# Kernel tuning notes

Hardware: AMD Instinct MI355X
Metric: run time of the kernel (lower is better)

## Reference

```python
import jax, jax.numpy as jnp
import numpy as np

B, N, K = 4, 1024, 512
HEADS, DH = 8, 64
HID = 2048
KAPPA = 1.0      # kappa_beta
ALPHA = 1e-3     # ffn_alpha (prior weight)
LAM = 1.0        # ffn_lambda_belief
NITER = 2        # ffn_n_iterations
EPS = 1e-8


def _ln(x, g, b):
    m = jnp.mean(x, axis=-1, keepdims=True)
    v = jnp.var(x, axis=-1, keepdims=True)
    return (x - m) * jax.lax.rsqrt(v + 1e-5) * g + b


def _transport(x, phi, G):
    # truncated exp(phi . G) applied to x without materializing (B,N,K,K)
    def Ax(y):
        return jnp.einsum('bng,gkl,bnl->bnk', phi, G, y)
    a1 = Ax(x)
    return x + a1 + 0.5 * Ax(a1)


def setup_inputs() -> dict:
    key = jax.random.key(0)
    ks = jax.random.split(key, 16)
    mu_q = jax.random.normal(ks[0], (B, N, K), dtype=jnp.float32)
    sigma_q = jax.random.uniform(ks[1], (B, N, K), minval=0.5, maxval=1.5, dtype=jnp.float32)
    phi = 0.1 * jax.random.normal(ks[2], (B, N, 3), dtype=jnp.float32)
    A = jax.random.normal(ks[3], (3, K, K), dtype=jnp.float32)
    generators = 0.05 * (A - jnp.transpose(A, (0, 2, 1)))  # antisymmetric Lie generators
    mask = jnp.broadcast_to(jnp.tril(jnp.ones((N, N), dtype=bool)), (B, N, N))  # causal
    mu_prior = jax.random.normal(ks[4], (B, N, K), dtype=jnp.float32)
    s = 0.02
    Wq = s * jax.random.normal(ks[5], (K, K), dtype=jnp.float32)
    Wk = s * jax.random.normal(ks[6], (K, K), dtype=jnp.float32)
    Wv = s * jax.random.normal(ks[7], (K, K), dtype=jnp.float32)
    Wo = s * jax.random.normal(ks[8], (K, K), dtype=jnp.float32)
    g1 = jnp.ones((K,), jnp.float32); be1 = jnp.zeros((K,), jnp.float32)
    g2 = jnp.ones((K,), jnp.float32); be2 = jnp.zeros((K,), jnp.float32)
    W1 = s * jax.random.normal(ks[9], (K, HID), dtype=jnp.float32)
    bh1 = jnp.zeros((HID,), jnp.float32)
    W2 = s * jax.random.normal(ks[10], (HID, K), dtype=jnp.float32)
    bh2 = jnp.zeros((K,), jnp.float32)
    lr = jnp.array(0.1, jnp.float32)  # learnable VFE step size
    return {'mu_q': mu_q, 'sigma_q': sigma_q, 'phi': phi, 'generators': generators,
            'mask': mask, 'mu_prior': mu_prior, 'Wq': Wq, 'Wk': Wk, 'Wv': Wv, 'Wo': Wo,
            'g1': g1, 'be1': be1, 'g2': g2, 'be2': be2,
            'W1': W1, 'bh1': bh1, 'W2': W2, 'bh2': bh2, 'lr': lr}


def reference(mu_q, sigma_q, phi, generators, mask, mu_prior,
              Wq, Wk, Wv, Wo, g1, be1, g2, be2, W1, bh1, W2, bh2, lr):
    # ---- attention sublayer ----
    mu_n = _ln(mu_q, g1, be1)
    mu_g = _transport(mu_n, phi, generators)  # transport to common frame

    def heads(x):  # (B,N,K) -> (B,H,N,Dh)
        return x.reshape(B, N, HEADS, DH).transpose(0, 2, 1, 3)

    q = heads(mu_g @ Wq)
    k = heads(mu_g @ Wk)
    v = heads(mu_g @ Wv)
    # diagonal covariance propagated through linear maps: var_out = sigma @ W^2
    sq = heads(sigma_q @ (Wq * Wq)) + EPS
    sk = heads(sigma_q @ (Wk * Wk)) + EPS

    inv = 1.0 / sq
    # KL(N(k_j,sk_j) || N(q_i,sq_i)) for diagonal Gaussians, decomposed into matmuls
    tr = jnp.einsum('bhid,bhjd->bhij', inv, sk)
    quad = (jnp.sum(q * q * inv, axis=-1)[..., None]
            - 2.0 * jnp.einsum('bhid,bhjd->bhij', q * inv, k)
            + jnp.einsum('bhid,bhjd->bhij', inv, k * k))
    logdet = (jnp.sum(jnp.log(sq), axis=-1)[..., None]
              - jnp.sum(jnp.log(sk), axis=-1)[:, :, None, :])
    kl = 0.5 * (tr + quad - DH + logdet)  # (B,H,N,N)

    scores = jnp.where(mask[:, None, :, :], -kl / KAPPA, -1e9)
    beta = jax.nn.softmax(scores, axis=-1)

    out = jnp.einsum('bhij,bhjd->bhid', beta, v)
    out = out.transpose(0, 2, 1, 3).reshape(B, N, K)
    mu_attn = _transport(out @ Wo, -phi, generators)  # back-transport to local frames
    mu_res = mu_q + mu_attn  # residual (dropout is identity in eval)

    # ---- VFE_dynamic FFN sublayer ----
    mu_n2 = _ln(mu_res, g2, be2)
    beta_m = jnp.mean(beta, axis=1)  # (B,N,N) attention-belief coupling
    h = mu_n2
    for _ in range(NITER):
        drive = jax.nn.gelu(h @ W1 + bh1) @ W2 + bh2
        grad = ALPHA * (h - mu_prior) + LAM * (h - jnp.einsum('bij,bjk->bik', beta_m, h))
        h = h + lr * (drive - grad)
    mu_out = mu_res + (h - mu_n2)

    return (mu_out, sigma_q, phi)
```

## Files before the change

kernel.cpp:

```cpp
#include <hip/hip_runtime.h>
#include <math.h>

#define BB 4
#define NN 1024
#define KK 512
#define HH 8
#define DHh 64
#define HIDd 2048
#define BN (BB*NN)

typedef unsigned short u16;
typedef __attribute__((ext_vector_type(8))) short bf16x8;
typedef __attribute__((ext_vector_type(4))) float f32x4;

__device__ __forceinline__ float gelu_tanh(float x){
    float u = 0.7978845608028654f*(x + 0.044715f*x*x*x);
    u = fminf(fmaxf(u, -15.f), 15.f);
    float t = __expf(2.f*u);
    return x*t/(t+1.f);
}
__device__ __forceinline__ u16 f2bf(float x){
    unsigned int u = __float_as_uint(x);
    unsigned int r = (u + 0x7fffu + ((u>>16)&1u)) >> 16;
    return (u16)r;
}
__device__ __forceinline__ float bf2f(u16 b){
    return __uint_as_float(((unsigned int)b)<<16);
}
__device__ __forceinline__ void gload16(const void* g, void* l){
    __builtin_amdgcn_global_load_lds((__attribute__((address_space(1))) void*)g,
                                     (__attribute__((address_space(3))) void*)l, 16, 0, 0);
}
__device__ __forceinline__ void wsplit(u16* hi, u16* lo, size_t o, float v){
    u16 h = f2bf(v);
    hi[o] = h;
    if (lo) lo[o] = f2bf(v - bf2f(h));
}

__global__ __launch_bounds__(256) void split_t_k(
    const float* __restrict__ src, u16* __restrict__ hi, u16* __restrict__ lo,
    int Kc, int Nc, long sS, long sD, int square)
{
    __shared__ float t[32][33];
    const int n0 = blockIdx.x*32, k0 = blockIdx.y*32, bz = blockIdx.z;
    const float* S = src + (long)bz*sS;
    const int tx = threadIdx.x & 31, ty = threadIdx.x >> 5;
    for (int r = ty; r < 32; r += 8){
        float v = S[(long)(k0+r)*Nc + n0+tx];
        if (square) v *= v;
        t[r][tx] = v;
    }
    __syncthreads();
    for (int r = ty; r < 32; r += 8){
        float v = t[tx][r];
        long o = (long)bz*sD + (long)(n0+r)*Kc + k0 + tx;
        wsplit(hi, lo, o, v);
    }
}

__global__ __launch_bounds__(256) void wmega_k(
    const float* __restrict__ Wq, const float* __restrict__ Wk,
    const float* __restrict__ Wv, const float* __restrict__ Wo,
    const float* __restrict__ W1, const float* __restrict__ W2,
    const float* __restrict__ gen,
    u16* __restrict__ WQKVh, u16* __restrict__ WQKVl, u16* __restrict__ WoTh,
    u16* __restrict__ WSQKh, u16* __restrict__ WSQKl,
    u16* __restrict__ W1Th, u16* __restrict__ W2Th, u16* __restrict__ GFh)
{
    const int z = blockIdx.z;
    const int tid = threadIdx.x;
    if (z == 8){
        if (blockIdx.x >= 48) return;
        const int c0 = blockIdx.x*32, k0 = blockIdx.y*32;
        const int tx = tid&31, ty = tid>>5;
        const int g = c0/KK, l0 = c0%KK;
        for (int r=ty; r<32; r+=8)
            GFh[(size_t)(k0+r)*(3*KK) + c0+tx] =
                f2bf(gen[(size_t)g*KK*KK + (size_t)(k0+r)*KK + l0+tx]);
        return;
    }
    __shared__ float t[32][33];
    const float* src; u16* hi; u16* lo=0; int sq=0;
    int n0, k0, Kc, Nc;
    const size_t KK2 = (size_t)KK*KK;
    if (z < 6){
        if (blockIdx.x >= 16) return;
        n0 = blockIdx.x*32; k0 = blockIdx.y*32; Kc=KK; Nc=KK;
        if      (z==0){ src=Wq; hi=WQKVh;       lo=WQKVl; }
        else if (z==1){ src=Wk; hi=WQKVh+KK2;   lo=WQKVl+KK2; }
        else if (z==2){ src=Wv; hi=WQKVh+2*KK2; lo=WQKVl+2*KK2; }
        else if (z==3){ src=Wo; hi=WoTh; }
        else if (z==4){ src=Wq; hi=WSQKh;       lo=WSQKl; sq=1; }
        else          { src=Wk; hi=WSQKh+KK2;   lo=WSQKl+KK2; sq=1; }
    } else if (z == 6){
        src=W1; hi=W1Th; Kc=KK; Nc=HIDd;
        n0 = blockIdx.x*32; k0 = blockIdx.y*32;
    } else {
        src=W2; hi=W2Th; Kc=HIDd; Nc=KK;
        n0 = blockIdx.y*32; k0 = blockIdx.x*32;
    }
    const int tx=tid&31, ty=tid>>5;
    for (int r=ty;r<32;r+=8){
        float v = src[(long)(k0+r)*Nc + n0+tx];
        if (sq) v*=v;
        t[r][tx]=v;
    }
    __syncthreads();
    for (int r=ty;r<32;r+=8){
        float v = t[tx][r];
        long o = (long)(n0+r)*Kc + k0+tx;
        wsplit(hi, lo, o, v);
    }
}

__global__ __launch_bounds__(256) void gemm_mfma_k(
    const u16* __restrict__ Ah, const u16* __restrict__ Bh,
    float* __restrict__ C, u16* __restrict__ Chi, u16* __restrict__ Clo,
    int M, int Kc, int Nc, int lda,
    long sA, long sB, long sC, const float* __restrict__ bias, int act,
    int swz,
    const u16* __restrict__ A2, const u16* __restrict__ B2,
    float* __restrict__ C2, int ycut)
{
    __shared__ u16 shA[3][128*32], shB[3][128*32];
    int bx = blockIdx.x, by = blockIdx.y;
    if (swz){
        int lin = bx + gridDim.x*by;
        int within = lin & 31, st = lin >> 5;
        int stm = gridDim.x >> 3;
        bx = (st % stm)*8 + (within & 7);
        by = (st / stm)*4 + (within >> 3);
    }
    int bz = blockIdx.z;
    int m0, n0, kend;
    const u16 *gAh, *gBh;
    if (ycut && by < ycut){
        m0 = (bx & 7)*128; n0 = by*128; bz = bx >> 3;
        gAh = A2 + (long)bz*NN*NN;
        gBh = B2 + (long)bz*KK*NN;
        Kc = NN; lda = NN; Nc = KK;
        C = C2 + (long)bz*NN*KK; Chi = 0; Clo = 0; bias = 0; act = 0; sC = 0;
        kend = m0 + 128;
        bz = 0;
    } else {
        if (ycut) by -= ycut;
        m0 = bx*128; n0 = by*128;
        gAh = Ah + (long)bz*sA;
        gBh = Bh + (long)bz*sB;
        kend = Kc;
    }
    const int tid = threadIdx.x;
    const int wave = tid >> 6, lane = tid & 63;
    const int quad = lane >> 4, r16 = lane & 15;
    const int wm = (wave>>1)*64, wn = (wave&1)*64;

    f32x4 acc[4][4];
    #pragma unroll
    for (int i=0;i<4;i++)
        #pragma unroll
        for (int j=0;j<4;j++) acc[i][j] = (f32x4){0.f,0.f,0.f,0.f};

    auto stage = [&](int sel, int k0){
        #pragma unroll
        for (int half=0; half<2; ++half){
            int c = half*256 + tid;
            int row = c >> 2;
            int kg = ((c & 3) ^ ((row >> 1) & 3))*8;
            gload16(gAh + (long)(m0+row)*lda + k0 + kg, &shA[sel][c*8]);
            gload16(gBh + (long)(n0+row)*Kc  + k0 + kg, &shB[sel][c*8]);
        }
    };

    const int nsteps = kend >> 5;
    stage(0, 0);
    if (1 < nsteps) stage(1, 1<<5);
    const int swr = (quad ^ ((r16 >> 1) & 3))*8;
    for (int t = 0; t < nsteps; ++t){
        if (t+1 < nsteps) asm volatile("s_waitcnt vmcnt(4)" ::: "memory");
        else              asm volatile("s_waitcnt vmcnt(0)" ::: "memory");
        __builtin_amdgcn_s_barrier();
        if (t+2 < nsteps) stage((t+2)%3, (t+2)<<5);
        const int rd = t % 3;
        bf16x8 afh[4], bfh[4];
        #pragma unroll
        for (int i=0;i<4;i++){
            afh[i] = *(const bf16x8*)&shA[rd][(wm+i*16+r16)*32 + swr];
            bfh[i] = *(const bf16x8*)&shB[rd][(wn+i*16+r16)*32 + swr];
        }
        #pragma unroll
        for (int i=0;i<4;i++)
            #pragma unroll
            for (int j=0;j<4;j++)
                acc[i][j] = __builtin_amdgcn_mfma_f32_16x16x32_bf16(afh[i], bfh[j], acc[i][j], 0,0,0);
    }
    #pragma unroll
    for (int i=0;i<4;i++){
        #pragma unroll
        for (int j=0;j<4;j++){
            int gc = n0 + wn + j*16 + r16;
            if (gc >= Nc) continue;
            float bv = bias ? bias[gc] : 0.f;
            #pragma unroll
            for (int r=0;r<4;r++){
                long gr = m0 + wm + i*16 + quad*4 + r;
                float v = acc[i][j][r] + bv;
                if (act) v = gelu_tanh(v);
                long o = (long)bz*sC + gr*Nc + gc;
                if (C) C[o] = v;
                if (Chi){ u16 t = f2bf(v); Chi[o] = t; if (Clo) Clo[o] = f2bf(v - bf2f(t)); }
            }
        }
    }
}

template<int NBUF>
__global__ __launch_bounds__(256) void gemm_v3_k(
    const u16* __restrict__ Ah, const u16* __restrict__ Al,
    const u16* __restrict__ Bh, const u16* __restrict__ Bl,
    float* __restrict__ C,
    int M, int Kc, int Nc, int lda,
    long sA, long sB, long sC, int cskip, int swzmode,
    const u16* __restrict__ Ah2, const u16* __restrict__ Al2,
    const u16* __restrict__ Bh2, const u16* __restrict__ Bl2,
    float* __restrict__ C2, int ycut, int Nc2,
    const float* __restrict__ dvec)
{
    __shared__ u16 shA[NBUF][128*32], shB[NBUF][128*32];
    int bx = blockIdx.x, by = blockIdx.y, bz = blockIdx.z;
    if (swzmode == 1){
        int lin = bx + gridDim.x*by;
        int within = lin & 31, st = lin >> 5;
        int stm = gridDim.x >> 3;
        bx = (st % stm)*8 + (within & 7);
        by = (st / stm)*4 + (within >> 3);
    } else if (swzmode == 2){
        int lin = bx + gridDim.x*(by + gridDim.y*bz);
        int xcd = lin & 7, idx = lin >> 3;
        bz = xcd + 8*(idx >> 6);
        int tile = idx & 63;
        bx = tile & 7; by = tile >> 3;
    }
    if (ycut && by >= ycut){
        Ah = Ah2; Al = Al2; Bh = Bh2; Bl = Bl2; C = C2;
        by -= ycut; Nc = Nc2;
    }
    const int m0 = bx*128, n0 = by*128;
    if (cskip == 1 && n0 > m0 + 127) return;
    const u16* gAh = Ah + (long)bz*sA;
    const u16* gAl = Al + (long)bz*sA;
    const u16* gBh = Bh + (long)bz*sB;
    const u16* gBl = Bl + (long)bz*sB;
    const int tid = threadIdx.x;
    const int wave = tid >> 6, lane = tid & 63;
    const int quad = lane >> 4, r16 = lane & 15;
    const int wm = (wave>>1)*64, wn = (wave&1)*64;

    f32x4 acc[4][4];
    #pragma unroll
    for (int i=0;i<4;i++)
        #pragma unroll
        for (int j=0;j<4;j++) acc[i][j] = (f32x4){0.f,0.f,0.f,0.f};

    const int segsteps = Kc >> 5;
    const int nsteps = 3*segsteps;
    auto stage = [&](int sel, int t){
        int seg = (t >= segsteps) + (t >= 2*segsteps);
        int k0 = (t - seg*segsteps) << 5;
        const u16* a = (seg==1) ? gAl : gAh;
        const u16* b = (seg==2) ? gBl : gBh;
        #pragma unroll
        for (int half=0; half<2; ++half){
            int c = half*256 + tid;
            int row = c >> 2;
            int kg = ((c & 3) ^ ((row >> 1) & 3))*8;
            gload16(a + (long)(m0+row)*lda + k0 + kg, &shA[sel][c*8]);
            gload16(b + (long)(n0+row)*Kc  + k0 + kg, &shB[sel][c*8]);
        }
    };

    const int swr = (quad ^ ((r16 >> 1) & 3))*8;
    if constexpr (NBUF == 2){
        stage(0, 0);
        __syncthreads();
        int cur = 0;
        for (int t = 0; t < nsteps; ++t){
            if (t+1 < nsteps) stage(cur^1, t+1);
            bf16x8 afh[4], bfh[4];
            #pragma unroll
            for (int i=0;i<4;i++){
                afh[i] = *(const bf16x8*)&shA[cur][(wm+i*16+r16)*32 + swr];
                bfh[i] = *(const bf16x8*)&shB[cur][(wn+i*16+r16)*32 + swr];
            }
            #pragma unroll
            for (int i=0;i<4;i++)
                #pragma unroll
                for (int j=0;j<4;j++)
                    acc[i][j] = __builtin_amdgcn_mfma_f32_16x16x32_bf16(afh[i], bfh[j], acc[i][j], 0,0,0);
            __syncthreads();
            cur ^= 1;
        }
    } else {
        stage(0, 0);
        if (1 < nsteps) stage(1, 1);
        for (int t = 0; t < nsteps; ++t){
            if (t+1 < nsteps) asm volatile("s_waitcnt vmcnt(4)" ::: "memory");
            else              asm volatile("s_waitcnt vmcnt(0)" ::: "memory");
            __builtin_amdgcn_s_barrier();
            if (t+2 < nsteps) stage((t+2)%3, t+2);
            const int rd = t % 3;
            bf16x8 afh[4], bfh[4];
            #pragma unroll
            for (int i=0;i<4;i++){
                afh[i] = *(const bf16x8*)&shA[rd][(wm+i*16+r16)*32 + swr];
                bfh[i] = *(const bf16x8*)&shB[rd][(wn+i*16+r16)*32 + swr];
            }
            #pragma unroll
            for (int i=0;i<4;i++)
                #pragma unroll
                for (int j=0;j<4;j++)
                    acc[i][j] = __builtin_amdgcn_mfma_f32_16x16x32_bf16(afh[i], bfh[j], acc[i][j], 0,0,0);
        }
    }
    float dv4[4];
    if (dvec){
        #pragma unroll
        for (int j=0;j<4;j++)
            dv4[j] = 0.5f*dvec[(size_t)bz*NN + n0 + wn + j*16 + r16];
    }
    #pragma unroll
    for (int i=0;i<4;i++){
        #pragma unroll
        for (int j=0;j<4;j++){
            int gc = n0 + wn + j*16 + r16;
            if (gc >= Nc) continue;
            #pragma unroll
            for (int r=0;r<4;r++){
                long gr = m0 + wm + i*16 + quad*4 + r;
                if (cskip == 1 && gc > gr) continue;
                long o = (long)bz*sC + gr*Nc + gc;
                float v = acc[i][j][r];
                if (dvec) v = -0.5f*v + dv4[j];
                C[o] = v;
            }
        }
    }
}

__global__ __launch_bounds__(256) void tgemm_k(
    const u16* __restrict__ Ahh,
    const u16* __restrict__ GFh,
    const float* __restrict__ phi, float esign,
    float* __restrict__ C, u16* __restrict__ Chi, u16* __restrict__ Clo,
    const float* __restrict__ t_x, const float* __restrict__ t_a1,
    const float* __restrict__ t_res)
{
    __shared__ u16 shA[2][64*64], shB[2][64*64];
    const int m0 = blockIdx.x*64, n0 = blockIdx.y*64;
    const int tid = threadIdx.x;
    const int wave = tid >> 6, lane = tid & 63;
    const int quad = lane >> 4, r16 = lane & 15;
    const int wr = wave*16;

    float ph[3][4];
    #pragma unroll
    for (int sgi=0; sgi<3; ++sgi)
        #pragma unroll
        for (int r=0; r<4; ++r)
            ph[sgi][r] = esign*phi[(size_t)(m0+wr+quad*4+r)*3 + sgi];

    f32x4 acc[4], tot[4];
    #pragma unroll
    for (int j=0;j<4;j++){ acc[j] = (f32x4){0.f,0.f,0.f,0.f}; tot[j] = acc[j]; }

    auto stage = [&](int sel, int t){
        int seg = t >> 3, k0 = (t & 7) << 6;
        #pragma unroll
        for (int rep=0; rep<2; ++rep){
            int c = rep*256 + tid;
            int row = c >> 3;
            int kg = ((c & 7) ^ (row & 7))*8;
            gload16(Ahh + (long)(m0+row)*KK + k0 + kg, &shA[sel][c*8]);
            gload16(GFh + (long)(n0+row)*(3*KK) + seg*KK + k0 + kg, &shB[sel][c*8]);
        }
    };

    stage(0, 0);
    __syncthreads();
    int cur = 0;
    for (int t = 0; t < 24; ++t){
        if (t+1 < 24) stage(cur^1, t+1);
        #pragma unroll
        for (int kk=0; kk<2; ++kk){
            const int s = (((kk<<2)+quad) ^ (r16 & 7))*8;
            bf16x8 af = *(const bf16x8*)&shA[cur][(wr+r16)*64 + s];
            #pragma unroll
            for (int j=0;j<4;j++){
                bf16x8 bh = *(const bf16x8*)&shB[cur][(j*16+r16)*64 + s];
                acc[j] = __builtin_amdgcn_mfma_f32_16x16x32_bf16(af, bh, acc[j], 0,0,0);
            }
        }
        if ((t & 7) == 7){
            int sgi = t >> 3;
            #pragma unroll
            for (int j=0;j<4;j++){
                #pragma unroll
                for (int r=0;r<4;r++) tot[j][r] += ph[sgi][r]*acc[j][r];
                acc[j] = (f32x4){0.f,0.f,0.f,0.f};
            }
        }
        __syncthreads();
        cur ^= 1;
    }
    #pragma unroll
    for (int j=0;j<4;j++){
        int gc = n0 + j*16 + r16;
        #pragma unroll
        for (int r=0;r<4;r++){
            long gr = m0 + wr + quad*4 + r;
            float v = tot[j][r];
            long o = gr*(long)KK + gc;
            if (t_x){
                v = t_x[o] + t_a1[o] + 0.5f*v;
                if (t_res) v += t_res[o];
            }
            if (C) C[o] = v;
            if (Chi){ u16 t2 = f2bf(v); Chi[o] = t2; if (Clo) Clo[o] = f2bf(v - bf2f(t2)); }
        }
    }
}

__global__ __launch_bounds__(256) void gemm64_k(
    const u16* __restrict__ Ah, const u16* __restrict__ Bh,
    float* __restrict__ C, u16* __restrict__ Chi, u16* __restrict__ Clo,
    int M, int Kc, int Nc, int lda,
    long sA, long sB, long sC, const float* __restrict__ bias, int act,
    int ktrim, int swz,
    const float* __restrict__ f_hin, const float* __restrict__ f_bmh,
    const float* __restrict__ f_mup, const float* __restrict__ f_lr,
    u16* __restrict__ f_hh, float* __restrict__ f_hout,
    const float* __restrict__ f_mrb, const float* __restrict__ f_mn2,
    float* __restrict__ f_out, int fmode)
{
    __shared__ u16 shA[2][64*64], shB[2][64*64];
    int bx = blockIdx.x, by = blockIdx.y;
    if (swz){
        int lin = bx + gridDim.x*by;
        int within = lin & 31, st = lin >> 5;
        int stm = gridDim.x >> 3;
        bx = (st % stm)*8 + (within & 7);
        by = (st / stm)*4 + (within >> 3);
    }
    const int m0 = bx*64, n0 = by*64;
    const int bz = blockIdx.z;
    const u16* gA = Ah + (long)bz*sA;
    const u16* gB = Bh + (long)bz*sB;
    const int tid = threadIdx.x;
    const int wave = tid >> 6, lane = tid & 63;
    const int quad = lane >> 4, r16 = lane & 15;
    const int wr = wave*16;
    const int kend = ktrim ? min(Kc, m0 + 64) : Kc;
    const int nsteps = kend >> 6;

    f32x4 acc[4];
    #pragma unroll
    for (int j=0;j<4;j++) acc[j] = (f32x4){0.f,0.f,0.f,0.f};

    auto stage = [&](int sel, int k0){
        #pragma unroll
        for (int rep=0; rep<2; ++rep){
            int c = rep*256 + tid;
            int row = c >> 3;
            int kg = ((c & 7) ^ (row & 7))*8;
            gload16(gA + (long)(m0+row)*lda + k0 + kg, &shA[sel][c*8]);
            gload16(gB + (long)(n0+row)*Kc + k0 + kg, &shB[sel][c*8]);
        }
    };

    stage(0, 0);
    __syncthreads();
    int cur = 0;
    for (int t = 0; t < nsteps; ++t){
        if (t+1 < nsteps) stage(cur^1, (t+1)<<6);
        #pragma unroll
        for (int kk=0; kk<2; ++kk){
            const int s = (((kk<<2)+quad) ^ (r16 & 7))*8;
            bf16x8 af = *(const bf16x8*)&shA[cur][(wr+r16)*64 + s];
            #pragma unroll
            for (int j=0;j<4;j++){
                bf16x8 bh = *(const bf16x8*)&shB[cur][(j*16+r16)*64 + s];
                acc[j] = __builtin_amdgcn_mfma_f32_16x16x32_bf16(af, bh, acc[j], 0,0,0);
            }
        }
        __syncthreads();
        cur ^= 1;
    }
    float lrv = 0.f;
    if (fmode) lrv = *f_lr;
    #pragma unroll
    for (int j=0;j<4;j++){
        int gc = n0 + j*16 + r16;
        float bv = bias ? bias[gc] : 0.f;
        #pragma unroll
        for (int r=0;r<4;r++){
            long gr = m0 + wr + quad*4 + r;
            float v = acc[j][r] + bv;
            if (act) v = gelu_tanh(v);
            long o = (long)bz*sC + gr*Nc + gc;
            if (fmode){
                float hv = f_hin[o];
                float val = hv + lrv*(v - (1e-3f*(hv - f_mup[o]) + (hv - f_bmh[o])));
                if (fmode == 1){ f_hout[o] = val; f_hh[o] = f2bf(val); }
                else           { f_out[o] = f_mrb[o] + val - f_mn2[o]; }
            } else {
                if (C) C[o] = v;
                if (Chi){ u16 t = f2bf(v); Chi[o] = t; if (Clo) Clo[o] = f2bf(v - bf2f(t)); }
            }
        }
    }
}

__global__ __launch_bounds__(256) void ln_k(
    const float* __restrict__ x, const float* __restrict__ g,
    const float* __restrict__ be, float* __restrict__ y,
    u16* __restrict__ yh16,
    const float* __restrict__ sg, u16* __restrict__ sgh, u16* __restrict__ sgl,
    float* __restrict__ osig, const float* __restrict__ phi, float* __restrict__ ophi)
{
    __shared__ float sh[8];
    const int r = blockIdx.x, tid = threadIdx.x;
    const float* xr = x + (long)r*KK;
    float2 v = *(const float2*)(xr + tid*2);
    float s = v.x+v.y, s2 = v.x*v.x+v.y*v.y;
    #pragma unroll
    for (int o=32;o>0;o>>=1){ s += __shfl_down(s,o); s2 += __shfl_down(s2,o); }
    if ((tid&63)==0){ sh[tid>>6]=s; sh[4+(tid>>6)]=s2; }
    __syncthreads();
    s  = sh[0]+sh[1]+sh[2]+sh[3];
    s2 = sh[4]+sh[5]+sh[6]+sh[7];
    const float mean = s*(1.f/KK);
    const float var  = s2*(1.f/KK) - mean*mean;
    const float rs = rsqrtf(var + 1e-5f);
    float2 gg = *(const float2*)(g + tid*2);
    float2 bb = *(const float2*)(be + tid*2);
    float ox = (v.x-mean)*rs*gg.x + bb.x;
    float oy = (v.y-mean)*rs*gg.y + bb.y;
    long o = (long)r*KK + tid*2;
    *(float2*)(y + o) = make_float2(ox, oy);
    if (yh16){ yh16[o] = f2bf(ox); yh16[o+1] = f2bf(oy); }
    if (sgh){
        float2 sv = *(const float2*)(sg + o);
        wsplit(sgh, sgl, o,   sv.x);
        wsplit(sgh, sgl, o+1, sv.y);
        if (osig) *(float2*)(osig + o) = sv;
    }
    if (ophi && tid < 3) ophi[(size_t)r*3 + tid] = phi[(size_t)r*3 + tid];
}

__global__ __launch_bounds__(512) void prepvt_k(
    const float* __restrict__ QKV, const float* __restrict__ SQSK,
    u16* __restrict__ CFh, u16* __restrict__ CFl,
    u16* __restrict__ KSh, u16* __restrict__ KSl, float* __restrict__ dvec,
    u16* __restrict__ VTh)
{
    __shared__ float t[64][65];
    const int bx = blockIdx.x;
    const int tid = threadIdx.x;
    if (bx < BN){
        const int bn = bx;
        const int b = bn / NN, n = bn % NN;
        const int h = tid >> 6, d = tid & 63;
        float q  = QKV[(size_t)bn*1536 + h*DHh + d];
        float k  = QKV[(size_t)bn*1536 + KK + h*DHh + d];
        float sq = SQSK[(size_t)bn*1024 + h*DHh + d] + 1e-8f;
        float sk = SQSK[(size_t)bn*1024 + KK + h*DHh + d] + 1e-8f;
        float inv = 1.f/sq;
        float nqi = -2.f*q*inv;
        float skk = sk + k*k;
        const size_t base = ((size_t)(h*BB + b)*NN + n)*128;
        wsplit(CFh, CFl, base+d,    inv);
        wsplit(CFh, CFl, base+64+d, nqi);
        wsplit(KSh, KSl, base+d,    skk);
        wsplit(KSh, KSl, base+64+d, k);
        float dv = __logf(sk);
        #pragma unroll
        for (int o=32;o>0;o>>=1) dv += __shfl_down(dv,o);
        if (d==0) dvec[((size_t)h*BB + b)*NN + n] = dv;
        return;
    }
    const int idx = bx - BN;
    const int n0 = (idx & 15)*64;
    const int h = (idx>>4)&7;
    const int b = idx>>7;
    const int c4 = (tid & 15) * 4;
    const int r0 = tid >> 4;
    for (int rr = r0; rr < 64; rr += 32){
        float4 v = *(const float4*)(QKV + (size_t)(b*NN + n0 + rr)*1536 + 1024 + h*DHh + c4);
        t[c4+0][rr] = v.x; t[c4+1][rr] = v.y; t[c4+2][rr] = v.z; t[c4+3][rr] = v.w;
    }
    __syncthreads();
    for (int dd = r0; dd < 64; dd += 32){
        size_t base = ((size_t)(h*BB + b)*64 + dd)*NN + n0 + c4;
        #pragma unroll
        for (int q=0;q<4;q++) VTh[base+q] = f2bf(t[dd][c4+q]);
    }
}

__global__ __launch_bounds__(256) void softmax_all_k(
    float* __restrict__ S, u16* __restrict__ BMh)
{
    __shared__ float s_redA[2][4], s_redB[2][4];
    const int tid = threadIdx.x;
    const int b = blockIdx.x >> 10, i = blockIdx.x & (NN-1);
    const int L = i + 1;
    const int JEND = ((i >> 6) + 1) << 6;
    const int JEND2 = ((i >> 7) + 1) << 7;
    const int j4 = tid*4;
    const bool act = (j4 < JEND);
    const int wv = tid >> 6;
    const bool lane0 = ((tid & 63) == 0);

    float bm[4] = {0.f,0.f,0.f,0.f};
    float4 rv = make_float4(0,0,0,0);
    if (act) rv = *(const float4*)(S + ((long)(0*BB + b)*NN + i)*NN + j4);
    for (int h = 0; h < 8; ++h){
        const int z = h*BB + b;
        float4 rvn = make_float4(0,0,0,0);
        if (h < 7 && act){
            const int zn = (h+1)*BB + b;
            rvn = *(const float4*)(S + ((long)zn*NN + i)*NN + j4);
        }
        float sc[4];
        const float* rp = (const float*)&rv;
        #pragma unroll
        for (int e=0;e<4;e++)
            sc[e] = (act && (j4 + e < L)) ? rp[e] : -3.0e38f;
        float lm = fmaxf(fmaxf(sc[0],sc[1]), fmaxf(sc[2],sc[3]));
        #pragma unroll
        for (int o=32;o>0;o>>=1) lm = fmaxf(lm, __shfl_xor(lm, o));
        if (lane0) s_redA[h&1][wv] = lm;
        __syncthreads();
        const float mx = fmaxf(fmaxf(s_redA[h&1][0],s_redA[h&1][1]),
                               fmaxf(s_redA[h&1][2],s_redA[h&1][3]));
        float w4[4], ps = 0.f;
        #pragma unroll
        for (int e=0;e<4;e++){
            float e1 = (act && (j4 + e < L)) ? __expf(sc[e]-mx) : 0.f;
            w4[e] = e1; ps += e1;
        }
        #pragma unroll
        for (int o=32;o>0;o>>=1) ps += __shfl_xor(ps, o);
        if (lane0) s_redB[h&1][wv] = ps;
        __syncthreads();
        const float isum = 1.f/(s_redB[h&1][0]+s_redB[h&1][1]+s_redB[h&1][2]+s_redB[h&1][3]);
        if (act){
            u16* brow = (u16*)(S + ((long)z*NN + i)*NN);
            ushort4 st;
            float w0=w4[0]*isum, w1=w4[1]*isum, w2=w4[2]*isum, w3=w4[3]*isum;
            bm[0]+=0.125f*w0; bm[1]+=0.125f*w1; bm[2]+=0.125f*w2; bm[3]+=0.125f*w3;
            st.x=f2bf(w0); st.y=f2bf(w1); st.z=f2bf(w2); st.w=f2bf(w3);
            *(ushort4*)(brow + j4) = st;
        }
        rv = rvn;
    }
    if (j4 < JEND2){
        const long bmrow = ((long)b*NN + i)*NN;
        ushort4 st;
        st.x=f2bf(bm[0]); st.y=f2bf(bm[1]); st.z=f2bf(bm[2]); st.w=f2bf(bm[3]);
        *(ushort4*)(BMh + bmrow + j4) = st;
    }
}

__global__ __launch_bounds__(256) void pv_k(
    const u16* __restrict__ Sbeta,
    const u16* __restrict__ VTh,
    u16* __restrict__ xh)
{
    __shared__ u16 shA[2][64*64], shB[2][64*64];
    const int m0 = blockIdx.x*64;
    const int z = blockIdx.y;
    const int b = z & 3, head = z >> 2;
    const int tid = threadIdx.x;
    const int wave = tid>>6, lane = tid&63;
    const int quad = lane>>4, r16 = lane&15;
    f32x4 acc[4];
    #pragma unroll
    for (int j=0;j<4;j++) acc[j]=(f32x4){0.f,0.f,0.f,0.f};
    const int nsteps = (m0 >> 6) + 1;

    auto stage = [&](int sel, int j0){
        #pragma unroll
        for (int rep=0; rep<2; ++rep){
            int c = rep*256 + tid;
            int row = c >> 3;
            int k8 = ((c & 7) ^ (row & 7))*8;
            gload16(Sbeta + ((size_t)(z*NN + m0 + row))*(2*NN) + j0 + k8, &shA[sel][c*8]);
            gload16(VTh + ((size_t)(z*64 + row))*NN + j0 + k8, &shB[sel][c*8]);
        }
    };

    stage(0, 0);
    __syncthreads();
    int cur = 0;
    for (int t = 0; t < nsteps; ++t){
        if (t+1 < nsteps) stage(cur^1, (t+1)<<6);
        #pragma unroll
        for (int kk=0; kk<2; ++kk){
            const int s = (((kk<<2)+quad) ^ (r16 & 7))*8;
            bf16x8 af = *(const bf16x8*)&shA[cur][(wave*16 + r16)*64 + s];
            #pragma unroll
            for (int nj=0; nj<4; ++nj){
                bf16x8 bh = *(const bf16x8*)&shB[cur][(nj*16 + r16)*64 + s];
                acc[nj] = __builtin_amdgcn_mfma_f32_16x16x32_bf16(af, bh, acc[nj], 0,0,0);
            }
        }
        __syncthreads();
        cur ^= 1;
    }
    #pragma unroll
    for (int nj=0;nj<4;nj++){
        #pragma unroll
        for (int r=0;r<4;r++){
            int i = m0 + wave*16 + quad*4 + r;
            int d = nj*16 + r16;
            size_t o = ((size_t)(b*NN)+i)*KK + head*64 + d;
            xh[o] = f2bf(acc[nj][r]);
        }
    }
}

extern "C" void kernel_launch(void* const* d_in, const int* in_sizes, int n_in,
                              void* d_out, int out_size, void* d_ws, size_t ws_size,
                              hipStream_t stream) {
    const float* mu_q    = (const float*)d_in[0];
    const float* sigma_q = (const float*)d_in[1];
    const float* phi     = (const float*)d_in[2];
    const float* gen     = (const float*)d_in[3];
    const float* mu_prior= (const float*)d_in[5];
    const float* Wq = (const float*)d_in[6];
    const float* Wk = (const float*)d_in[7];
    const float* Wv = (const float*)d_in[8];
    const float* Wo = (const float*)d_in[9];
    const float* g1 = (const float*)d_in[10];
    const float* be1= (const float*)d_in[11];
    const float* g2 = (const float*)d_in[12];
    const float* be2= (const float*)d_in[13];
    const float* W1 = (const float*)d_in[14];
    const float* bh1= (const float*)d_in[15];
    const float* W2 = (const float*)d_in[16];
    const float* bh2= (const float*)d_in[17];
    const float* lr = (const float*)d_in[18];
    float* out = (float*)d_out;

    float* w = (float*)d_ws;
    size_t off = 0;
    auto alloc = [&](size_t n){ float* p = w + off; off += (n+3)&~(size_t)3; return p; };
    auto ualloc = [&](size_t n){ return (u16*)alloc((n+1)/2); };

    float* Xb   = alloc((size_t)BN*KK);
    float* A1b  = alloc((size_t)BN*KK);
    float* A2b  = alloc((size_t)BN*KK);
    float* QKVb = alloc((size_t)BN*3*KK);
    float* SQSKb= alloc((size_t)BN*2*KK);
    float* REG  = alloc((size_t)16*NN*NN);
    float* Sbig = Xb;
    u16*  SGh   = (u16*)REG;
    u16*  SGl   = SGh + (size_t)BN*KK;
    u16*  Xh    = SGl + (size_t)BN*KK;
    u16*  A1h   = Xh  + (size_t)BN*KK;
    u16*  WOh   = A1h + (size_t)BN*KK;
    u16*  ZH    = (u16*)REG;
    float* Db_  = alloc((size_t)HH*BB*NN);
    u16* AH  = ualloc((size_t)BN*HIDd); u16* AL  = ualloc((size_t)BN*HIDd);
    u16* CFh = AH;
    u16* CFl = AH + (size_t)HH*BB*NN*128;
    u16* KSh = AL;
    u16* KSl = AL + (size_t)HH*BB*NN*128;
    u16* VTh = ualloc((size_t)HH*BB*64*NN);
    u16* GFh = ualloc((size_t)3*KK*KK);
    u16* WQKVh= ualloc((size_t)3*KK*KK); u16* WQKVl= ualloc((size_t)3*KK*KK);
    u16* WSQKh= ualloc((size_t)2*KK*KK); u16* WSQKl= ualloc((size_t)2*KK*KK);
    u16* WoTh= ualloc((size_t)KK*KK);
    u16* W1Th= ualloc((size_t)KK*HIDd);
    u16* W2Th= ualloc((size_t)KK*HIDd);
    u16* BMh = ualloc((size_t)BB*NN*NN);
    u16* HTh = ualloc((size_t)BB*KK*NN);
    float* WOb = QKVb;
    float* Hb  = QKVb + (size_t)BN*KK;
    float* MRb = QKVb + 2*(size_t)BN*KK;
    float* MN2b= Xb;
    (void)A2b;

    {
        dim3 gw(64, 16, 9);
        wmega_k<<<gw, 256, 0, stream>>>(Wq, Wk, Wv, Wo, W1, W2, gen,
                                        WQKVh, WQKVl, WoTh, WSQKh, WSQKl,
                                        W1Th, W2Th, GFh);
    }

    ln_k<<<BN, 256, 0, stream>>>(mu_q, g1, be1, Xb, Xh, sigma_q, SGh, SGl,
                                 out + (size_t)BN*KK, phi, out + 2*(size_t)BN*KK);
    {
        dim3 tg(BN/64, KK/64, 1);
        tgemm_k<<<tg, 256, 0, stream>>>(Xh, GFh, phi, 1.f, A1b, A1h, 0, 0, 0, 0);
        tgemm_k<<<tg, 256, 0, stream>>>(A1h, GFh, phi, 1.f, 0, AH, AL, Xb, A1b, 0);
    }

    {
        dim3 g(BN/128, 20, 1);
        gemm_v3_k<3><<<g, 256, 0, stream>>>(AH, AL, WQKVh, WQKVl, QKVb,
            BN, KK, 3*KK, KK, 0, 0, 0, 0, 1,
            SGh, SGl, WSQKh, WSQKl, SQSKb, 12, 2*KK, 0);
    }
    prepvt_k<<<BN + 512, 512, 0, stream>>>(QKVb, SQSKb, CFh, CFl, KSh, KSl, Db_, VTh);

    {
        dim3 sg(NN/128, NN/128, 32);
        gemm_v3_k<2><<<sg, 256, 0, stream>>>(CFh, CFl, KSh, KSl, Sbig,
            NN, 128, NN, 128, (long)NN*128, (long)NN*128, (long)NN*NN, 1, 2,
            0, 0, 0, 0, 0, 0, 0, Db_);
        softmax_all_k<<<BB*NN, 256, 0, stream>>>(Sbig, BMh);
        dim3 pg(NN/64, 32, 1);
        pv_k<<<pg, 256, 0, stream>>>((const u16*)Sbig, VTh, AH);
    }

    {
        dim3 wg(BN/64, KK/64, 1);
        gemm64_k<<<wg, 256, 0, stream>>>(AH, WoTh, WOb, WOh, 0,
            BN, KK, KK, KK, 0,0,0, nullptr, 0, 0, 0,
            0,0,0,0,0,0,0,0,0,0);
        dim3 tg(BN/64, KK/64, 1);
        tgemm_k<<<tg, 256, 0, stream>>>(WOh, GFh, phi, -1.f, A1b, A1h, 0, 0, 0, 0);
        tgemm_k<<<tg, 256, 0, stream>>>(A1h, GFh, phi, -1.f, MRb, 0, 0, WOb, A1b, mu_q);
    }
    ln_k<<<BN, 256, 0, stream>>>(MRb, g2, be2, MN2b, AH, 0, 0, 0, 0, 0, 0);

    for (int it=0; it<2; ++it){
        const float* hin = (it==0) ? MN2b : Hb;
        {
            dim3 tg(KK/32, NN/32, BB);
            split_t_k<<<tg, 256, 0, stream>>>(hin, HTh, 0, NN, KK,
                                              (long)NN*KK, (long)KK*NN, 0);
        }
        {
            dim3 wg1(BN/128, 4 + HIDd/128, 1);
            gemm_mfma_k<<<wg1, 256, 0, stream>>>(AH, W1Th, 0, ZH, 0,
                BN, KK, HIDd, KK, 0, 0, 0, bh1, 1, 1,
                BMh, HTh, A1b, 4);
        }
        {
            dim3 wg(BN/64, KK/64, 1);
            gemm64_k<<<wg, 256, 0, stream>>>(ZH, W2Th, 0,0,0,
                                             BN, HIDd, KK, HIDd, 0,0,0, bh2, 0, 0, 1,
                                             hin, A1b, mu_prior, lr, AH, Hb, MRb, MN2b, out,
                                             (it==0) ? 1 : 2);
        }
    }

    (void)in_sizes; (void)n_in; (void)out_size; (void)ws_size;
}
```

Baseline: 540.8 us.

## Triple-buffer LDS staging with explicit vmcnt waits in bf16 GEMM kernels

Both the transport GEMM and the general 64x64 GEMM move from double to triple LDS buffering, prefetching two k-steps ahead. Each step now waits with an explicit s_waitcnt vmcnt and a single barrier instead of two __syncthreads, so global loads overlap more with MFMA work and there is one barrier per step. The cost is 50% more LDS per block, which may lower occupancy. Correctness also depends on the vmcnt(4) count matching the number of async loads issued per stage.

```diff
diff --git a/kernel.cpp b/kernel.cpp
--- a/kernel.cpp
+++ b/kernel.cpp
@@ -354,7 +354,7 @@
     const float* __restrict__ t_x, const float* __restrict__ t_a1,
     const float* __restrict__ t_res)
 {
-    __shared__ u16 shA[2][64*64], shB[2][64*64];
+    __shared__ u16 shA[3][64*64], shB[3][64*64];
     const int m0 = blockIdx.x*64, n0 = blockIdx.y*64;
     const int tid = threadIdx.x;
     const int wave = tid >> 6, lane = tid & 63;
@@ -385,17 +385,20 @@
     };
 
     stage(0, 0);
-    __syncthreads();
-    int cur = 0;
+    stage(1, 1);
     for (int t = 0; t < 24; ++t){
-        if (t+1 < 24) stage(cur^1, t+1);
+        if (t+1 < 24) asm volatile("s_waitcnt vmcnt(4)" ::: "memory");
+        else          asm volatile("s_waitcnt vmcnt(0)" ::: "memory");
+        __builtin_amdgcn_s_barrier();
+        if (t+2 < 24) stage((t+2)%3, t+2);
+        const int rd = t % 3;
         #pragma unroll
         for (int kk=0; kk<2; ++kk){
             const int s = (((kk<<2)+quad) ^ (r16 & 7))*8;
-            bf16x8 af = *(const bf16x8*)&shA[cur][(wr+r16)*64 + s];
+            bf16x8 af = *(const bf16x8*)&shA[rd][(wr+r16)*64 + s];
             #pragma unroll
             for (int j=0;j<4;j++){
-                bf16x8 bh = *(const bf16x8*)&shB[cur][(j*16+r16)*64 + s];
+                bf16x8 bh = *(const bf16x8*)&shB[rd][(j*16+r16)*64 + s];
                 acc[j] = __builtin_amdgcn_mfma_f32_16x16x32_bf16(af, bh, acc[j], 0,0,0);
             }
         }
@@ -408,8 +411,6 @@
                 acc[j] = (f32x4){0.f,0.f,0.f,0.f};
             }
         }
-        __syncthreads();
-        cur ^= 1;
     }
     #pragma unroll
     for (int j=0;j<4;j++){
@@ -441,7 +442,7 @@
     const float* __restrict__ f_mrb, const float* __restrict__ f_mn2,
     float* __restrict__ f_out, int fmode)
 {
-    __shared__ u16 shA[2][64*64], shB[2][64*64];
+    __shared__ u16 shA[3][64*64], shB[3][64*64];
     int bx = blockIdx.x, by = blockIdx.y;
     if (swz){
         int lin = bx + gridDim.x*by;
@@ -477,22 +478,23 @@
     };
 
     stage(0, 0);
-    __syncthreads();
-    int cur = 0;
+    if (1 < nsteps) stage(1, 1<<6);
     for (int t = 0; t < nsteps; ++t){
-        if (t+1 < nsteps) stage(cur^1, (t+1)<<6);
+        if (t+1 < nsteps) asm volatile("s_waitcnt vmcnt(4)" ::: "memory");
+        else              asm volatile("s_waitcnt vmcnt(0)" ::: "memory");
+        __builtin_amdgcn_s_barrier();
+        if (t+2 < nsteps) stage((t+2)%3, (t+2)<<6);
+        const int rd = t % 3;
         #pragma unroll
         for (int kk=0; kk<2; ++kk){
             const int s = (((kk<<2)+quad) ^ (r16 & 7))*8;
-            bf16x8 af = *(const bf16x8*)&shA[cur][(wr+r16)*64 + s];
+            bf16x8 af = *(const bf16x8*)&shA[rd][(wr+r16)*64 + s];
             #pragma unroll
             for (int j=0;j<4;j++){
-                bf16x8 bh = *(const bf16x8*)&shB[cur][(j*16+r16)*64 + s];
+                bf16x8 bh = *(const bf16x8*)&shB[rd][(j*16+r16)*64 + s];
                 acc[j] = __builtin_amdgcn_mfma_f32_16x16x32_bf16(af, bh, acc[j], 0,0,0);
             }
         }
-        __syncthreads();
-        cur ^= 1;
     }
     float lrv = 0.f;
     if (fmode) lrv = *f_lr;
```

New measurement: 523.9 us. 1.03x faster.
